# Kernel optimization log

Measured on AMD Instinct MI355X. Metric: run time of the kernel, lower is better.

The kernel has to match this reference:

```python
import jax, jax.numpy as jnp
import numpy as np

H, W, C = 96, 96, 21
THETA_ALPHA, THETA_BETA, THETA_GAMMA = 8.0, 0.125, 3.0
NUM_ITERATIONS = 5


def setup_inputs() -> dict:
    key = jax.random.key(0)
    k1, k2, k3, k4, k5 = jax.random.split(key, 5)
    unaries = jax.random.normal(k1, (1, H, W, C), dtype=jnp.float32)
    reference_image = jax.random.uniform(k2, (1, H, W, 3), dtype=jnp.float32)
    # truncated normal(mean=0, std=0.1) as in tf.initializers.truncated_normal
    spatial_ker_weights = 0.1 * jax.random.truncated_normal(k3, -2.0, 2.0, (C,), dtype=jnp.float32)
    bilateral_ker_weights = 0.1 * jax.random.truncated_normal(k4, -2.0, 2.0, (C,), dtype=jnp.float32)
    compatibility_matrix = 0.1 * jax.random.truncated_normal(k5, -2.0, 2.0, (C, C), dtype=jnp.float32)
    return {
        "unaries": unaries,
        "reference_image": reference_image,
        "spatial_ker_weights": spatial_ker_weights,
        "bilateral_ker_weights": bilateral_ker_weights,
        "compatibility_matrix": compatibility_matrix,
    }


def _gaussian_kernel(feats):
    # feats: [B, N, D] -> K[b, i, j] = exp(-0.5 * ||f_i - f_j||^2)
    sq = jnp.sum(feats * feats, axis=-1)  # [B, N]
    d2 = sq[:, :, None] + sq[:, None, :] - 2.0 * jnp.einsum("bnd,bmd->bnm", feats, feats)
    return jnp.exp(-0.5 * jnp.maximum(d2, 0.0))


def _build_kernels(reference_image):
    # Exact-math equivalent of the permutohedral lattice Gaussian filter:
    # spatial features = positions/theta_gamma; bilateral = [pos/theta_alpha, rgb/theta_beta].
    B = reference_image.shape[0]
    yy, xx = jnp.meshgrid(jnp.arange(H, dtype=jnp.float32), jnp.arange(W, dtype=jnp.float32), indexing="ij")
    pos = jnp.stack([yy, xx], axis=-1).reshape(1, H * W, 2)  # [1, N, 2]
    pos = jnp.broadcast_to(pos, (B, H * W, 2))
    col = reference_image.reshape(B, H * W, 3)
    k_spatial = _gaussian_kernel(pos / THETA_GAMMA)
    k_bilateral = _gaussian_kernel(jnp.concatenate([pos / THETA_ALPHA, col / THETA_BETA], axis=-1))
    return k_spatial, k_bilateral


def reference(unaries, reference_image, spatial_ker_weights, bilateral_ker_weights, compatibility_matrix):
    B = unaries.shape[0]
    N = H * W
    k_spatial, k_bilateral = _build_kernels(reference_image)  # built once; reused each iteration
    u = unaries.reshape(B, N, C)
    q = u
    for _ in range(NUM_ITERATIONS):
        q = jax.nn.softmax(q, axis=-1)
        spatial_out = jnp.einsum("bnm,bmc->bnc", k_spatial, q)
        bilateral_out = jnp.einsum("bnm,bmc->bnc", k_bilateral, q)
        # pairwise^T = compat @ diag(w_s) @ S^T + compat @ diag(w_b) @ Bi^T
        # => pairwise = (S * w_s + Bi * w_b) @ compat^T
        message = spatial_out * spatial_ker_weights + bilateral_out * bilateral_ker_weights
        pairwise = message @ compatibility_matrix.T
        q = u - pairwise
    return q.reshape(unaries.shape)
```

## Files before the change

kernel.cpp:

```cpp
#include <hip/hip_runtime.h>
#include <hip/hip_bf16.h>
#include <algorithm>
#include <cmath>

#define HH 96
#define WW 96
#define CC 21
#define NN (HH*WW)
#define NELEM (NN*CC)
#define RS 20
#define NPAR (2*CC + CC*CC)
#define L2E 1.4426950408889634f
#define MSTEPS 24
#define NBB (36*24)
#define NSTRIP 8
#define NBLUR (CC*NSTRIP)
#define SROWS 12
#define TRUNC2 1225
#define BLURKEY 0x10000

typedef short bf16x8 __attribute__((ext_vector_type(8)));
typedef float f32x16 __attribute__((ext_vector_type(16)));

__device__ __forceinline__ float fexp2(float x) { return __builtin_amdgcn_exp2f(x); }
__device__ __forceinline__ float fexp(float x)  { return __builtin_amdgcn_exp2f(x * L2E); }

__device__ __forceinline__ short f2b(float f) {
    __hip_bfloat16 h = __float2bfloat16(f);
    short s; __builtin_memcpy(&s, &h, 2); return s;
}

__global__ void k_sniff(const unsigned short* __restrict__ u16, int* __restrict__ flag32) {
    __shared__ int sfound;
    if (threadIdx.x == 0) sfound = 0;
    __syncthreads();
    const int base = blockIdx.x * (NELEM/32);
    int found = 0;
    for (int i = base + threadIdx.x; i < base + NELEM/32; i += 256) {
        unsigned v = u16[i];
        if ((v & 0x7F80u) == 0x7F80u) found = 1;
    }
    if (found) sfound = 1;
    __syncthreads();
    if (threadIdx.x == 0) flag32[blockIdx.x] = sfound;
}

__device__ __forceinline__ int rdflag(const int* __restrict__ flag32) {
    int f = 0;
    #pragma unroll
    for (int i = 0; i < 32; i++) f |= flag32[i];
    return f;
}

__global__ __launch_bounds__(256) void k_prep(
    const void* __restrict__ u, const void* __restrict__ img,
    const void* __restrict__ wS, const void* __restrict__ wB,
    const void* __restrict__ compat, const int* __restrict__ flag32,
    float* __restrict__ uf, float* __restrict__ featx, float* __restrict__ par,
    float* __restrict__ bil, __hip_bfloat16* __restrict__ pT)
{
    const int f = rdflag(flag32);
    const int tid = threadIdx.x;
    const int n = blockIdx.x * 256 + tid;

    if (blockIdx.x == 0) {
        for (int i = tid; i < NPAR; i += 256) {
            const void* src; int j;
            if (i < CC)        { src = wS;     j = i; }
            else if (i < 2*CC) { src = wB;     j = i - CC; }
            else               { src = compat; j = i - 2*CC; }
            par[i] = f ? ((const float*)src)[j]
                       : __bfloat162float(((const __hip_bfloat16*)src)[j]);
        }
    }

    {
        float c0, c1, c2;
        if (f) { const float* p = (const float*)img;
                 c0 = p[3*n]; c1 = p[3*n+1]; c2 = p[3*n+2]; }
        else   { const __hip_bfloat16* p = (const __hip_bfloat16*)img;
                 c0 = __bfloat162float(p[3*n]); c1 = __bfloat162float(p[3*n+1]);
                 c2 = __bfloat162float(p[3*n+2]); }
        float ym = (float)(n / WW), xm = (float)(n % WW);
        const float sc = 0.15014029f;
        const float cf = 9.6089787f;
        featx[8*n + 0] = -L2E * (fmaf(ym, ym, xm*xm) * 0.0078125f
                                 + 32.f * (c0*c0 + c1*c1 + c2*c2));
        featx[8*n + 1] = sc * ym;
        featx[8*n + 2] = sc * xm;
        featx[8*n + 3] = cf * c0;
        featx[8*n + 4] = cf * c1;
        featx[8*n + 5] = cf * c2;
        featx[8*n + 6] = 0.f;
        featx[8*n + 7] = 0.f;
    }

    float v[CC];
    float mx = -1e30f;
    #pragma unroll
    for (int c = 0; c < CC; c++) {
        float uv = f ? ((const float*)u)[n*CC + c]
                     : __bfloat162float(((const __hip_bfloat16*)u)[n*CC + c]);
        uf[n*CC + c] = uv;
        v[c] = uv;
        mx = fmaxf(mx, uv);
    }
    float s = 0.f;
    #pragma unroll
    for (int c = 0; c < CC; c++) { v[c] = fexp(v[c] - mx); s += v[c]; }
    float inv = 1.f / s;
    #pragma unroll
    for (int c = 0; c < CC; c++) {
        pT[(size_t)c*NN + n] = __float2bfloat16(v[c] * inv);
        bil[(size_t)c*NN + n] = 0.f;
    }
}

__global__ __launch_bounds__(256) void k_work(
    const __hip_bfloat16* __restrict__ pT,
    const float* __restrict__ featx,
    float* __restrict__ bil,
    float* __restrict__ s2T,
    const int* __restrict__ tab)
{
    __shared__ float smem[6176];
    const int tid = threadIdx.x;
    const int item = tab[blockIdx.x];

    if (item < BLURKEY) {
        float* lds_h = smem;
        const int wv   = tid >> 6, lane = tid & 63;
        const int quad = lane >> 5, lid = lane & 31;

        const int nt = item >> 5, mc = item & 31;
        const int ny0 = (nt / 6) * 16, nx0 = (nt % 6) * 16;
        const int my0 = (mc & 3) * 24, mx0 = (mc >> 2) * 16;

        const int dx = (mx0 > nx0 + 15) ? mx0 - (nx0 + 15)
                     : ((nx0 > mx0 + 15) ? nx0 - (mx0 + 15) : 0);
        const int lim = TRUNC2 - dx * dx;
        int T = (int)sqrtf((float)lim);
        T -= (T * T > lim);
        T += ((T + 1) * (T + 1) <= lim);

        int blo = ny0 - T - my0;      blo = blo < 0 ? 0 : blo;
        int bhi = ny0 + 15 + T - my0; bhi = bhi > 23 ? 23 : bhi;

        {
            float4* dst = (float4*)lds_h;
            for (int i = blo * 32 + tid; i < (bhi + 1) * 32; i += 256) {
                const int seg = i >> 5, off = i & 31;
                dst[i] = ((const float4*)(featx +
                          (size_t)((my0 + seg) * WW + mx0) * 8))[off];
            }
        }
        __syncthreads();

        const int by0 = ny0 + 4 * wv;
        int lo = by0 - T - my0;     lo = lo < 0 ? 0 : lo;
        int hi = by0 + 3 + T - my0; hi = hi > 23 ? 23 : hi;
        if (lo > hi) return;

        const int row = lid >> 4, col = lid & 15;
        const int n0 = (by0 + row) * WW + nx0 + col;
        const int n1 = n0 + 2 * WW;
        const float4 g0a = *(const float4*)(featx + (size_t)n0 * 8);
        const float4 g0b = *(const float4*)(featx + (size_t)n0 * 8 + 4);
        const float4 g1a = *(const float4*)(featx + (size_t)n1 * 8);
        const float4 g1b = *(const float4*)(featx + (size_t)n1 * 8 + 4);

        f32x16 acc0, acc1;
        #pragma unroll
        for (int r = 0; r < 16; r++) { acc0[r] = 0.f; acc1[r] = 0.f; }

        int mg = (my0 + lo) * WW + mx0 + quad * 8;
        #pragma unroll 1
        for (int step = lo; step <= hi; step++, mg += WW) {
            bf16x8 afrag = *(const bf16x8*)(pT + (size_t)lid * NN + mg);

            const float* h = lds_h + (step * 16 + quad * 8) * 8;
            float kb0[8], kb1[8];
            #pragma unroll
            for (int j = 0; j < 8; j++) {
                float4 ha = *(const float4*)(h + j * 8);
                float4 hb = *(const float4*)(h + j * 8 + 4);
                float s0 = g0a.x + ha.x;
                s0 = fmaf(g0a.y, ha.y, s0);
                s0 = fmaf(g0a.z, ha.z, s0);
                s0 = fmaf(g0a.w, ha.w, s0);
                s0 = fmaf(g0b.x, hb.x, s0);
                s0 = fmaf(g0b.y, hb.y, s0);
                kb0[j] = fexp2(s0);
                float s1 = g1a.x + ha.x;
                s1 = fmaf(g1a.y, ha.y, s1);
                s1 = fmaf(g1a.z, ha.z, s1);
                s1 = fmaf(g1a.w, ha.w, s1);
                s1 = fmaf(g1b.x, hb.x, s1);
                s1 = fmaf(g1b.y, hb.y, s1);
                kb1[j] = fexp2(s1);
            }
            bf16x8 b0, b1;
            #pragma unroll
            for (int j = 0; j < 8; j++) { b0[j] = f2b(kb0[j]); b1[j] = f2b(kb1[j]); }

            acc0 = __builtin_amdgcn_mfma_f32_32x32x16_bf16(afrag, b0, acc0, 0, 0, 0);
            acc1 = __builtin_amdgcn_mfma_f32_32x32x16_bf16(afrag, b1, acc1, 0, 0, 0);
        }

        #pragma unroll
        for (int r = 0; r < 16; r++) {
            int c = (r & 3) + 8 * (r >> 2) + 4 * quad;
            if (c < CC) {
                atomicAdd(&bil[(size_t)c * NN + n0], acc0[r]);
                atomicAdd(&bil[(size_t)c * NN + n1], acc1[r]);
            }
        }
    } else {
        __shared__ float w_s[RS + 1];
        float* A  = smem;
        float* B2 = smem + 4992;

        const int b2 = item - BLURKEY;
        const int c = b2 % CC;
        const int strip = b2 / CC;
        const int y0 = strip * SROWS;
        const int ylo = (y0 - RS < 0) ? 0 : y0 - RS;
        const int yhi = (y0 + SROWS - 1 + RS > HH - 1) ? HH - 1 : y0 + SROWS - 1 + RS;
        const int nrows = yhi - ylo + 1;

        if (tid <= RS) w_s[tid] = fexp2(-(float)(tid*tid) * (L2E / 18.f));
        const __hip_bfloat16* src = pT + (size_t)c * NN + ylo * WW;
        for (int i = tid; i < nrows * WW; i += 256)
            A[i] = __bfloat162float(src[i]);
        __syncthreads();

        for (int i = tid; i < SROWS * WW; i += 256) {
            const int yo = y0 + i / WW;
            const int x  = i % WW;
            float acc = A[(yo - ylo) * WW + x];
            #pragma unroll
            for (int d = 1; d <= RS; d++) {
                float s = 0.f;
                if (yo - d >= 0)  s += A[(yo - d - ylo) * WW + x];
                if (yo + d < HH)  s += A[(yo + d - ylo) * WW + x];
                acc = fmaf(w_s[d], s, acc);
            }
            B2[i] = acc;
        }
        __syncthreads();

        for (int i = tid; i < SROWS * WW; i += 256) {
            const int r = i / WW, x = i % WW;
            float acc = B2[i];
            #pragma unroll
            for (int d = 1; d <= RS; d++) {
                float s = 0.f;
                if (x - d >= 0)  s += B2[r * WW + x - d];
                if (x + d < WW)  s += B2[r * WW + x + d];
                acc = fmaf(w_s[d], s, acc);
            }
            s2T[(size_t)c * NN + (y0 + r) * WW + x] = acc;
        }
    }
}

__global__ __launch_bounds__(256) void k_update(
    float* __restrict__ bil, const float* __restrict__ s2T,
    const float* __restrict__ uf, const float* __restrict__ par,
    const int* __restrict__ flag32,
    __hip_bfloat16* __restrict__ pT, void* __restrict__ out, int last)
{
    __shared__ float sc[CC*CC + 1];
    __shared__ float sws[CC], swb[CC];
    const int tid = threadIdx.x;
    for (int i = tid; i < CC*CC; i += 256) sc[i] = par[2*CC + i];
    if (tid == 0) sc[CC*CC] = 0.f;
    if (tid < CC) { sws[tid] = par[tid]; swb[tid] = par[CC + tid]; }
    __syncthreads();

    const int half = tid & 1;
    const int n = blockIdx.x * 128 + (tid >> 1);

    float msg[11];
    #pragma unroll
    for (int k = 0; k < 11; k++) {
        const int cp = 2*k + half;
        if (cp < CC) {
            msg[k] = fmaf(s2T[(size_t)cp*NN + n], sws[cp],
                          bil[(size_t)cp*NN + n] * swb[cp]);
            bil[(size_t)cp*NN + n] = 0.f;
        } else msg[k] = 0.f;
    }

    float pw[CC];
    #pragma unroll
    for (int c = 0; c < CC; c++) {
        float a = msg[0] * sc[c*CC + half];
        #pragma unroll
        for (int k = 1; k < 11; k++)
            a = fmaf(msg[k], sc[c*CC + 2*k + half], a);
        pw[c] = a;
    }
    #pragma unroll
    for (int c = 0; c < CC; c++)
        pw[c] += __shfl_xor(pw[c], 1, 64);

    float qv[CC];
    float mx = -1e30f;
    #pragma unroll
    for (int c = 0; c < CC; c++) {
        qv[c] = uf[(size_t)n*CC + c] - pw[c];
        mx = fmaxf(mx, qv[c]);
    }

    if (last) {
        const int is_f32 = rdflag(flag32);
        #pragma unroll
        for (int k = 0; k < 11; k++) {
            const int ce = 2*k, co = (k < 10) ? 2*k + 1 : 0;
            float v = half ? qv[co] : qv[ce];
            const int c = 2*k + half;
            if (c < CC) {
                if (is_f32) ((float*)out)[(size_t)n*CC + c] = v;
                else ((__hip_bfloat16*)out)[(size_t)n*CC + c] = __float2bfloat16(v);
            }
        }
    } else {
        float ex[11]; float ssum = 0.f;
        #pragma unroll
        for (int k = 0; k < 11; k++) {
            const int ce = 2*k, co = (k < 10) ? 2*k + 1 : 0;
            float v = half ? qv[co] : qv[ce];
            float e = fexp(v - mx);
            if (2*k + half < CC) ssum += e;
            ex[k] = e;
        }
        ssum += __shfl_xor(ssum, 1, 64);
        const float inv = 1.f / ssum;
        #pragma unroll
        for (int k = 0; k < 11; k++) {
            const int c = 2*k + half;
            if (c < CC) pT[(size_t)c*NN + n] = __float2bfloat16(ex[k] * inv);
        }
    }
}

extern "C" void kernel_launch(void* const* d_in, const int* in_sizes, int n_in,
                              void* d_out, int out_size, void* d_ws, size_t ws_size,
                              hipStream_t stream)
{
    static int h_tab[NBB + NBLUR];
    static int h_n = 0;
    if (h_n == 0) {
        struct It { int key; int cost; };
        static It its[NBB + NBLUR];
        int m = 0;
        for (int nt = 0; nt < 36; nt++)
            for (int mc = 0; mc < 24; mc++) {
                const int ny0 = (nt / 6) * 16, nx0 = (nt % 6) * 16;
                const int my0 = (mc & 3) * 24, mx0 = (mc >> 2) * 16;
                const int dx = (mx0 > nx0 + 15) ? mx0 - (nx0 + 15)
                             : ((nx0 > mx0 + 15) ? nx0 - (mx0 + 15) : 0);
                const int lim = TRUNC2 - dx * dx;
                if (lim < 0) continue;
                int T = (int)std::sqrt((double)lim);
                while (T * T > lim) T--;
                while ((T + 1) * (T + 1) <= lim) T++;
                int cost = 0;
                for (int wv = 0; wv < 4; wv++) {
                    const int by0 = ny0 + 4 * wv;
                    int lo = by0 - T - my0;     if (lo < 0)  lo = 0;
                    int hi = by0 + 3 + T - my0; if (hi > 23) hi = 23;
                    if (lo <= hi) cost += hi - lo + 1;
                }
                if (cost == 0) continue;
                its[m].key = (nt << 5) | mc; its[m].cost = cost; m++;
            }
        for (int b = 0; b < NBLUR; b++) { its[m].key = BLURKEY + b; its[m].cost = 20; m++; }
        std::sort(its, its + m, [](const It& a, const It& b) { return a.cost > b.cost; });
        for (int i = 0; i < m; i++) h_tab[i] = its[i].key;
        h_n = m;
    }

    float* ws = (float*)d_ws;
    int*   flag32 = (int*)ws;
    float* par    = ws + 32;
    float* featx  = ws + 544;
    __hip_bfloat16* pT = (__hip_bfloat16*)(ws + 74272);
    float* uf  = ws + 74272 + 147456;
    float* s2T = uf + NELEM;
    float* bil = s2T + NELEM;
    int*   d_tab = (int*)(bil + NELEM);

    hipMemcpyAsync(d_tab, h_tab, h_n * sizeof(int), hipMemcpyHostToDevice, stream);

    k_sniff<<<32, 256, 0, stream>>>((const unsigned short*)d_in[0], flag32);
    k_prep<<<NN/256, 256, 0, stream>>>(d_in[0], d_in[1], d_in[2], d_in[3], d_in[4],
                                       flag32, uf, featx, par, bil, pT);

    for (int it = 0; it < 5; it++) {
        k_work<<<h_n, 256, 0, stream>>>(pT, featx, bil, s2T, d_tab);
        k_update<<<NN/128, 256, 0, stream>>>(bil, s2T, uf, par, flag32,
                                             pT, d_out, (it == 4) ? 1 : 0);
    }
}
```

Measured before the change: 237.9 us.

## Fuse all stages into one persistent cooperative kernel with grid syncs

Replaces the sniff, prep, and ten per-iteration work/update kernel launches with a single cooperative persistent kernel. Stages are separated by grid-wide barriers, and blocks loop over the work table and update chunks. The goal is to remove launch gaps and per-kernel ramp-up across the eleven small launches. In exchange, the grid is capped by occupancy (launch bounds 256,3), so work items are processed in loops instead of being fully spread across the device. Grid.sync also adds its own cost.

After: 574.5 us. 2.42x slower.

```diff
diff --git a/kernel.cpp b/kernel.cpp
--- a/kernel.cpp
+++ b/kernel.cpp
@@ -1,7 +1,10 @@
 #include <hip/hip_runtime.h>
+#include <hip/hip_cooperative_groups.h>
 #include <hip/hip_bf16.h>
 #include <algorithm>
 #include <cmath>
+
+namespace cg = cooperative_groups;
 
 #define HH 96
 #define WW 96
@@ -11,13 +14,12 @@
 #define RS 20
 #define NPAR (2*CC + CC*CC)
 #define L2E 1.4426950408889634f
-#define MSTEPS 24
 #define NBB (36*24)
-#define NSTRIP 8
-#define NBLUR (CC*NSTRIP)
+#define NBLUR (CC*8)
 #define SROWS 12
 #define TRUNC2 1225
 #define BLURKEY 0x10000
+#define NUPD (NN/128)
 
 typedef short bf16x8 __attribute__((ext_vector_type(8)));
 typedef float f32x16 __attribute__((ext_vector_type(16)));
@@ -30,318 +32,282 @@
     short s; __builtin_memcpy(&s, &h, 2); return s;
 }
 
-__global__ void k_sniff(const unsigned short* __restrict__ u16, int* __restrict__ flag32) {
-    __shared__ int sfound;
-    if (threadIdx.x == 0) sfound = 0;
-    __syncthreads();
-    const int base = blockIdx.x * (NELEM/32);
-    int found = 0;
-    for (int i = base + threadIdx.x; i < base + NELEM/32; i += 256) {
-        unsigned v = u16[i];
-        if ((v & 0x7F80u) == 0x7F80u) found = 1;
-    }
-    if (found) sfound = 1;
-    __syncthreads();
-    if (threadIdx.x == 0) flag32[blockIdx.x] = sfound;
-}
-
-__device__ __forceinline__ int rdflag(const int* __restrict__ flag32) {
+__global__ __launch_bounds__(256, 3) void k_all(
+    const void* __restrict__ u, const void* __restrict__ img,
+    const void* __restrict__ wS, const void* __restrict__ wB,
+    const void* __restrict__ compat, void* __restrict__ out,
+    float* __restrict__ uf, float* __restrict__ featx, float* __restrict__ par,
+    float* __restrict__ bil, __hip_bfloat16* __restrict__ pTg,
+    float* __restrict__ s2T, int* __restrict__ flag32,
+    const int* __restrict__ tab, int ntab)
+{
+    __shared__ float smem[6176];
+    cg::grid_group grid = cg::this_grid();
+    const int tid = threadIdx.x;
+    const int bid0 = blockIdx.x;
+    const int gsz = gridDim.x;
+
+    if (bid0 < 32) {
+        int* sf = (int*)smem;
+        if (tid == 0) *sf = 0;
+        __syncthreads();
+        const unsigned short* u16 = (const unsigned short*)u;
+        const int base = bid0 * (NELEM/32);
+        int found = 0;
+        for (int i = base + tid; i < base + NELEM/32; i += 256)
+            if ((u16[i] & 0x7F80u) == 0x7F80u) found = 1;
+        if (found) *sf = 1;
+        __syncthreads();
+        if (tid == 0) flag32[bid0] = *sf;
+    }
+    grid.sync();
+
     int f = 0;
     #pragma unroll
     for (int i = 0; i < 32; i++) f |= flag32[i];
-    return f;
-}
-
-__global__ __launch_bounds__(256) void k_prep(
-    const void* __restrict__ u, const void* __restrict__ img,
-    const void* __restrict__ wS, const void* __restrict__ wB,
-    const void* __restrict__ compat, const int* __restrict__ flag32,
-    float* __restrict__ uf, float* __restrict__ featx, float* __restrict__ par,
-    float* __restrict__ bil, __hip_bfloat16* __restrict__ pT)
-{
-    const int f = rdflag(flag32);
-    const int tid = threadIdx.x;
-    const int n = blockIdx.x * 256 + tid;
-
-    if (blockIdx.x == 0) {
-        for (int i = tid; i < NPAR; i += 256) {
-            const void* src; int j;
-            if (i < CC)        { src = wS;     j = i; }
-            else if (i < 2*CC) { src = wB;     j = i - CC; }
-            else               { src = compat; j = i - 2*CC; }
-            par[i] = f ? ((const float*)src)[j]
-                       : __bfloat162float(((const __hip_bfloat16*)src)[j]);
-        }
-    }
-
-    {
-        float c0, c1, c2;
-        if (f) { const float* p = (const float*)img;
-                 c0 = p[3*n]; c1 = p[3*n+1]; c2 = p[3*n+2]; }
-        else   { const __hip_bfloat16* p = (const __hip_bfloat16*)img;
-                 c0 = __bfloat162float(p[3*n]); c1 = __bfloat162float(p[3*n+1]);
-                 c2 = __bfloat162float(p[3*n+2]); }
-        float ym = (float)(n / WW), xm = (float)(n % WW);
-        const float sc = 0.15014029f;
-        const float cf = 9.6089787f;
-        featx[8*n + 0] = -L2E * (fmaf(ym, ym, xm*xm) * 0.0078125f
-                                 + 32.f * (c0*c0 + c1*c1 + c2*c2));
-        featx[8*n + 1] = sc * ym;
-        featx[8*n + 2] = sc * xm;
-        featx[8*n + 3] = cf * c0;
-        featx[8*n + 4] = cf * c1;
-        featx[8*n + 5] = cf * c2;
-        featx[8*n + 6] = 0.f;
-        featx[8*n + 7] = 0.f;
-    }
-
-    float v[CC];
-    float mx = -1e30f;
-    #pragma unroll
-    for (int c = 0; c < CC; c++) {
-        float uv = f ? ((const float*)u)[n*CC + c]
-                     : __bfloat162float(((const __hip_bfloat16*)u)[n*CC + c]);
-        uf[n*CC + c] = uv;
-        v[c] = uv;
-        mx = fmaxf(mx, uv);
-    }
-    float s = 0.f;
-    #pragma unroll
-    for (int c = 0; c < CC; c++) { v[c] = fexp(v[c] - mx); s += v[c]; }
-    float inv = 1.f / s;
-    #pragma unroll
-    for (int c = 0; c < CC; c++) {
-        pT[(size_t)c*NN + n] = __float2bfloat16(v[c] * inv);
-        bil[(size_t)c*NN + n] = 0.f;
-    }
-}
-
-__global__ __launch_bounds__(256) void k_work(
-    const __hip_bfloat16* __restrict__ pT,
-    const float* __restrict__ featx,
-    float* __restrict__ bil,
-    float* __restrict__ s2T,
-    const int* __restrict__ tab)
-{
-    __shared__ float smem[6176];
-    const int tid = threadIdx.x;
-    const int item = tab[blockIdx.x];
-
-    if (item < BLURKEY) {
-        float* lds_h = smem;
-        const int wv   = tid >> 6, lane = tid & 63;
-        const int quad = lane >> 5, lid = lane & 31;
-
-        const int nt = item >> 5, mc = item & 31;
-        const int ny0 = (nt / 6) * 16, nx0 = (nt % 6) * 16;
-        const int my0 = (mc & 3) * 24, mx0 = (mc >> 2) * 16;
-
-        const int dx = (mx0 > nx0 + 15) ? mx0 - (nx0 + 15)
-                     : ((nx0 > mx0 + 15) ? nx0 - (mx0 + 15) : 0);
-        const int lim = TRUNC2 - dx * dx;
-        int T = (int)sqrtf((float)lim);
-        T -= (T * T > lim);
-        T += ((T + 1) * (T + 1) <= lim);
-
-        int blo = ny0 - T - my0;      blo = blo < 0 ? 0 : blo;
-        int bhi = ny0 + 15 + T - my0; bhi = bhi > 23 ? 23 : bhi;
-
+
+    for (int ch = bid0; ch < 36; ch += gsz) {
+        const int n = ch * 256 + tid;
+        if (ch == 0) {
+            for (int i = tid; i < NPAR; i += 256) {
+                const void* src; int j;
+                if (i < CC)        { src = wS;     j = i; }
+                else if (i < 2*CC) { src = wB;     j = i - CC; }
+                else               { src = compat; j = i - 2*CC; }
+                par[i] = f ? ((const float*)src)[j]
+                           : __bfloat162float(((const __hip_bfloat16*)src)[j]);
+            }
+        }
         {
-            float4* dst = (float4*)lds_h;
-            for (int i = blo * 32 + tid; i < (bhi + 1) * 32; i += 256) {
-                const int seg = i >> 5, off = i & 31;
-                dst[i] = ((const float4*)(featx +
-                          (size_t)((my0 + seg) * WW + mx0) * 8))[off];
-            }
-        }
-        __syncthreads();
-
-        const int by0 = ny0 + 4 * wv;
-        int lo = by0 - T - my0;     lo = lo < 0 ? 0 : lo;
-        int hi = by0 + 3 + T - my0; hi = hi > 23 ? 23 : hi;
-        if (lo > hi) return;
-
-        const int row = lid >> 4, col = lid & 15;
-        const int n0 = (by0 + row) * WW + nx0 + col;
-        const int n1 = n0 + 2 * WW;
-        const float4 g0a = *(const float4*)(featx + (size_t)n0 * 8);
-        const float4 g0b = *(const float4*)(featx + (size_t)n0 * 8 + 4);
-        const float4 g1a = *(const float4*)(featx + (size_t)n1 * 8);
-        const float4 g1b = *(const float4*)(featx + (size_t)n1 * 8 + 4);
-
-        f32x16 acc0, acc1;
+            float c0, c1, c2;
+            if (f) { const float* p = (const float*)img;
+                     c0 = p[3*n]; c1 = p[3*n+1]; c2 = p[3*n+2]; }
+            else   { const __hip_bfloat16* p = (const __hip_bfloat16*)img;
+                     c0 = __bfloat162float(p[3*n]); c1 = __bfloat162float(p[3*n+1]);
+                     c2 = __bfloat162float(p[3*n+2]); }
+            float ym = (float)(n / WW), xm = (float)(n % WW);
+            const float sc_ = 0.15014029f;
+            const float cf  = 9.6089787f;
+            featx[8*n+0] = -L2E * (fmaf(ym, ym, xm*xm) * 0.0078125f
+                                   + 32.f * (c0*c0 + c1*c1 + c2*c2));
+            featx[8*n+1] = sc_*ym; featx[8*n+2] = sc_*xm;
+            featx[8*n+3] = cf*c0;  featx[8*n+4] = cf*c1;  featx[8*n+5] = cf*c2;
+            featx[8*n+6] = 0.f;    featx[8*n+7] = 0.f;
+        }
+        float v[CC]; float mx = -1e30f;
         #pragma unroll
-        for (int r = 0; r < 16; r++) { acc0[r] = 0.f; acc1[r] = 0.f; }
-
-        int mg = (my0 + lo) * WW + mx0 + quad * 8;
-        #pragma unroll 1
-        for (int step = lo; step <= hi; step++, mg += WW) {
-            bf16x8 afrag = *(const bf16x8*)(pT + (size_t)lid * NN + mg);
-
-            const float* h = lds_h + (step * 16 + quad * 8) * 8;
-            float kb0[8], kb1[8];
+        for (int c = 0; c < CC; c++) {
+            float uv = f ? ((const float*)u)[n*CC+c]
+                         : __bfloat162float(((const __hip_bfloat16*)u)[n*CC+c]);
+            uf[n*CC+c] = uv; v[c] = uv; mx = fmaxf(mx, uv);
+        }
+        float s = 0.f;
+        #pragma unroll
+        for (int c = 0; c < CC; c++) { v[c] = fexp(v[c]-mx); s += v[c]; }
+        float inv = 1.f/s;
+        #pragma unroll
+        for (int c = 0; c < CC; c++) {
+            pTg[(size_t)c*NN+n] = __float2bfloat16(v[c]*inv);
+            bil[(size_t)c*NN+n] = 0.f;
+        }
+    }
+    grid.sync();
+
+    for (int it = 0; it < 5; it++) {
+        for (int w = bid0; w < ntab; w += gsz) {
+            __syncthreads();
+            const int item = tab[w];
+            if (item < BLURKEY) {
+                float* lds_h = smem;
+                const int wv = tid >> 6, lane = tid & 63;
+                const int quad = lane >> 5, lid = lane & 31;
+                const int nt = item >> 5, mc = item & 31;
+                const int ny0 = (nt/6)*16, nx0 = (nt%6)*16;
+                const int my0 = (mc&3)*24, mx0 = (mc>>2)*16;
+                const int dx = (mx0 > nx0+15) ? mx0-(nx0+15)
+                             : ((nx0 > mx0+15) ? nx0-(mx0+15) : 0);
+                const int lim = TRUNC2 - dx*dx;
+                int T = (int)sqrtf((float)lim);
+                T -= (T*T > lim);
+                T += ((T+1)*(T+1) <= lim);
+                int blo = ny0 - T - my0;      blo = blo < 0 ? 0 : blo;
+                int bhi = ny0 + 15 + T - my0; bhi = bhi > 23 ? 23 : bhi;
+                {
+                    float4* dst = (float4*)lds_h;
+                    for (int i = blo*32 + tid; i < (bhi+1)*32; i += 256) {
+                        const int seg = i >> 5, off = i & 31;
+                        dst[i] = ((const float4*)(featx +
+                                  (size_t)((my0+seg)*WW + mx0)*8))[off];
+                    }
+                }
+                __syncthreads();
+                const int by0 = ny0 + 4*wv;
+                int lo = by0 - T - my0;     lo = lo < 0 ? 0 : lo;
+                int hi = by0 + 3 + T - my0; hi = hi > 23 ? 23 : hi;
+                if (lo <= hi) {
+                    const int row = lid >> 4, col = lid & 15;
+                    const int n0 = (by0+row)*WW + nx0 + col;
+                    const int n1 = n0 + 2*WW;
+                    const float4 g0a = *(const float4*)(featx + (size_t)n0*8);
+                    const float4 g0b = *(const float4*)(featx + (size_t)n0*8 + 4);
+                    const float4 g1a = *(const float4*)(featx + (size_t)n1*8);
+                    const float4 g1b = *(const float4*)(featx + (size_t)n1*8 + 4);
+                    f32x16 acc0, acc1;
+                    #pragma unroll
+                    for (int r = 0; r < 16; r++) { acc0[r]=0.f; acc1[r]=0.f; }
+                    int mg = (my0+lo)*WW + mx0 + quad*8;
+                    #pragma unroll 1
+                    for (int step = lo; step <= hi; step++, mg += WW) {
+                        bf16x8 afrag = *(const bf16x8*)(pTg + (size_t)lid*NN + mg);
+                        const float* h = lds_h + (step*16 + quad*8)*8;
+                        float kb0[8], kb1[8];
+                        #pragma unroll
+                        for (int j = 0; j < 8; j++) {
+                            float4 ha = *(const float4*)(h + j*8);
+                            float4 hb = *(const float4*)(h + j*8 + 4);
+                            float s0 = g0a.x + ha.x;
+                            s0 = fmaf(g0a.y,ha.y,s0); s0 = fmaf(g0a.z,ha.z,s0);
+                            s0 = fmaf(g0a.w,ha.w,s0); s0 = fmaf(g0b.x,hb.x,s0);
+                            s0 = fmaf(g0b.y,hb.y,s0);
+                            kb0[j] = fexp2(s0);
+                            float s1 = g1a.x + ha.x;
+                            s1 = fmaf(g1a.y,ha.y,s1); s1 = fmaf(g1a.z,ha.z,s1);
+                            s1 = fmaf(g1a.w,ha.w,s1); s1 = fmaf(g1b.x,hb.x,s1);
+                            s1 = fmaf(g1b.y,hb.y,s1);
+                            kb1[j] = fexp2(s1);
+                        }
+                        bf16x8 b0, b1;
+                        #pragma unroll
+                        for (int j = 0; j < 8; j++) { b0[j]=f2b(kb0[j]); b1[j]=f2b(kb1[j]); }
+                        acc0 = __builtin_amdgcn_mfma_f32_32x32x16_bf16(afrag,b0,acc0,0,0,0);
+                        acc1 = __builtin_amdgcn_mfma_f32_32x32x16_bf16(afrag,b1,acc1,0,0,0);
+                    }
+                    #pragma unroll
+                    for (int r = 0; r < 16; r++) {
+                        int c = (r&3) + 8*(r>>2) + 4*quad;
+                        if (c < CC) {
+                            atomicAdd(&bil[(size_t)c*NN + n0], acc0[r]);
+                            atomicAdd(&bil[(size_t)c*NN + n1], acc1[r]);
+                        }
+                    }
+                }
+            } else {
+                float* A   = smem;
+                float* B2  = smem + 4992;
+                float* w_s = smem + 6144;
+                const int b2 = item - BLURKEY;
+                const int c = b2 % CC;
+                const int strip = b2 / CC;
+                const int y0 = strip * SROWS;
+                const int ylo = (y0-RS < 0) ? 0 : y0-RS;
+                const int yhi = (y0+SROWS-1+RS > HH-1) ? HH-1 : y0+SROWS-1+RS;
+                const int nrows = yhi - ylo + 1;
+                if (tid <= RS) w_s[tid] = fexp2(-(float)(tid*tid)*(L2E/18.f));
+                const __hip_bfloat16* src = pTg + (size_t)c*NN + ylo*WW;
+                for (int i = tid; i < nrows*WW; i += 256)
+                    A[i] = __bfloat162float(src[i]);
+                __syncthreads();
+                for (int i = tid; i < SROWS*WW; i += 256) {
+                    const int yo = y0 + i/WW;
+                    const int x  = i % WW;
+                    float acc = A[(yo-ylo)*WW + x];
+                    #pragma unroll
+                    for (int d = 1; d <= RS; d++) {
+                        float s = 0.f;
+                        if (yo-d >= 0) s += A[(yo-d-ylo)*WW + x];
+                        if (yo+d < HH) s += A[(yo+d-ylo)*WW + x];
+                        acc = fmaf(w_s[d], s, acc);
+                    }
+                    B2[i] = acc;
+                }
+                __syncthreads();
+                for (int i = tid; i < SROWS*WW; i += 256) {
+                    const int r = i/WW, x = i%WW;
+                    float acc = B2[i];
+                    #pragma unroll
+                    for (int d = 1; d <= RS; d++) {
+                        float s = 0.f;
+                        if (x-d >= 0) s += B2[r*WW + x-d];
+                        if (x+d < WW) s += B2[r*WW + x+d];
+                        acc = fmaf(w_s[d], s, acc);
+                    }
+                    s2T[(size_t)c*NN + (y0+r)*WW + x] = acc;
+                }
+            }
+        }
+        grid.sync();
+
+        const int last = (it == 4);
+        for (int w = bid0; w < NUPD; w += gsz) {
+            __syncthreads();
+            float* sc  = smem;
+            float* sws = smem + 448;
+            float* swb = smem + 472;
+            for (int i = tid; i < CC*CC; i += 256) sc[i] = par[2*CC + i];
+            if (tid == 0) sc[CC*CC] = 0.f;
+            if (tid < CC) { sws[tid] = par[tid]; swb[tid] = par[CC+tid]; }
+            __syncthreads();
+            const int half = tid & 1;
+            const int n = w*128 + (tid >> 1);
+            float msg[11];
             #pragma unroll
-            for (int j = 0; j < 8; j++) {
-                float4 ha = *(const float4*)(h + j * 8);
-                float4 hb = *(const float4*)(h + j * 8 + 4);
-                float s0 = g0a.x + ha.x;
-                s0 = fmaf(g0a.y, ha.y, s0);
-                s0 = fmaf(g0a.z, ha.z, s0);
-                s0 = fmaf(g0a.w, ha.w, s0);
-                s0 = fmaf(g0b.x, hb.x, s0);
-                s0 = fmaf(g0b.y, hb.y, s0);
-                kb0[j] = fexp2(s0);
-                float s1 = g1a.x + ha.x;
-                s1 = fmaf(g1a.y, ha.y, s1);
-                s1 = fmaf(g1a.z, ha.z, s1);
-                s1 = fmaf(g1a.w, ha.w, s1);
-                s1 = fmaf(g1b.x, hb.x, s1);
-                s1 = fmaf(g1b.y, hb.y, s1);
-                kb1[j] = fexp2(s1);
-            }
-            bf16x8 b0, b1;
+            for (int k = 0; k < 11; k++) {
+                const int cp = 2*k + half;
+                if (cp < CC) {
+                    msg[k] = fmaf(s2T[(size_t)cp*NN+n], sws[cp],
+                                  bil[(size_t)cp*NN+n] * swb[cp]);
+                    bil[(size_t)cp*NN+n] = 0.f;
+                } else msg[k] = 0.f;
+            }
+            float pw[CC];
             #pragma unroll
-            for (int j = 0; j < 8; j++) { b0[j] = f2b(kb0[j]); b1[j] = f2b(kb1[j]); }
-
-            acc0 = __builtin_amdgcn_mfma_f32_32x32x16_bf16(afrag, b0, acc0, 0, 0, 0);
-            acc1 = __builtin_amdgcn_mfma_f32_32x32x16_bf16(afrag, b1, acc1, 0, 0, 0);
-        }
-
-        #pragma unroll
-        for (int r = 0; r < 16; r++) {
-            int c = (r & 3) + 8 * (r >> 2) + 4 * quad;
-            if (c < CC) {
-                atomicAdd(&bil[(size_t)c * NN + n0], acc0[r]);
-                atomicAdd(&bil[(size_t)c * NN + n1], acc1[r]);
-            }
-        }
-    } else {
-        __shared__ float w_s[RS + 1];
-        float* A  = smem;
-        float* B2 = smem + 4992;
-
-        const int b2 = item - BLURKEY;
-        const int c = b2 % CC;
-        const int strip = b2 / CC;
-        const int y0 = strip * SROWS;
-        const int ylo = (y0 - RS < 0) ? 0 : y0 - RS;
-        const int yhi = (y0 + SROWS - 1 + RS > HH - 1) ? HH - 1 : y0 + SROWS - 1 + RS;
-        const int nrows = yhi - ylo + 1;
-
-        if (tid <= RS) w_s[tid] = fexp2(-(float)(tid*tid) * (L2E / 18.f));
-        const __hip_bfloat16* src = pT + (size_t)c * NN + ylo * WW;
-        for (int i = tid; i < nrows * WW; i += 256)
-            A[i] = __bfloat162float(src[i]);
-        __syncthreads();
-
-        for (int i = tid; i < SROWS * WW; i += 256) {
-            const int yo = y0 + i / WW;
-            const int x  = i % WW;
-            float acc = A[(yo - ylo) * WW + x];
+            for (int c = 0; c < CC; c++) {
+                float a = msg[0] * sc[c*CC + half];
+                #pragma unroll
+                for (int k = 1; k < 11; k++)
+                    a = fmaf(msg[k], sc[c*CC + 2*k + half], a);
+                pw[c] = a;
+            }
             #pragma unroll
-            for (int d = 1; d <= RS; d++) {
-                float s = 0.f;
-                if (yo - d >= 0)  s += A[(yo - d - ylo) * WW + x];
-                if (yo + d < HH)  s += A[(yo + d - ylo) * WW + x];
-                acc = fmaf(w_s[d], s, acc);
-            }
-            B2[i] = acc;
-        }
-        __syncthreads();
-
-        for (int i = tid; i < SROWS * WW; i += 256) {
-            const int r = i / WW, x = i % WW;
-            float acc = B2[i];
+            for (int c = 0; c < CC; c++)
+                pw[c] += __shfl_xor(pw[c], 1, 64);
+            float qv[CC]; float mx = -1e30f;
             #pragma unroll
-            for (int d = 1; d <= RS; d++) {
-                float s = 0.f;
-                if (x - d >= 0)  s += B2[r * WW + x - d];
-                if (x + d < WW)  s += B2[r * WW + x + d];
-                acc = fmaf(w_s[d], s, acc);
-            }
-            s2T[(size_t)c * NN + (y0 + r) * WW + x] = acc;
-        }
-    }
-}
-
-__global__ __launch_bounds__(256) void k_update(
-    float* __restrict__ bil, const float* __restrict__ s2T,
-    const float* __restrict__ uf, const float* __restrict__ par,
-    const int* __restrict__ flag32,
-    __hip_bfloat16* __restrict__ pT, void* __restrict__ out, int last)
-{
-    __shared__ float sc[CC*CC + 1];
-    __shared__ float sws[CC], swb[CC];
-    const int tid = threadIdx.x;
-    for (int i = tid; i < CC*CC; i += 256) sc[i] = par[2*CC + i];
-    if (tid == 0) sc[CC*CC] = 0.f;
-    if (tid < CC) { sws[tid] = par[tid]; swb[tid] = par[CC + tid]; }
-    __syncthreads();
-
-    const int half = tid & 1;
-    const int n = blockIdx.x * 128 + (tid >> 1);
-
-    float msg[11];
-    #pragma unroll
-    for (int k = 0; k < 11; k++) {
-        const int cp = 2*k + half;
-        if (cp < CC) {
-            msg[k] = fmaf(s2T[(size_t)cp*NN + n], sws[cp],
-                          bil[(size_t)cp*NN + n] * swb[cp]);
-            bil[(size_t)cp*NN + n] = 0.f;
-        } else msg[k] = 0.f;
-    }
-
-    float pw[CC];
-    #pragma unroll
-    for (int c = 0; c < CC; c++) {
-        float a = msg[0] * sc[c*CC + half];
-        #pragma unroll
-        for (int k = 1; k < 11; k++)
-            a = fmaf(msg[k], sc[c*CC + 2*k + half], a);
-        pw[c] = a;
-    }
-    #pragma unroll
-    for (int c = 0; c < CC; c++)
-        pw[c] += __shfl_xor(pw[c], 1, 64);
-
-    float qv[CC];
-    float mx = -1e30f;
-    #pragma unroll
-    for (int c = 0; c < CC; c++) {
-        qv[c] = uf[(size_t)n*CC + c] - pw[c];
-        mx = fmaxf(mx, qv[c]);
-    }
-
-    if (last) {
-        const int is_f32 = rdflag(flag32);
-        #pragma unroll
-        for (int k = 0; k < 11; k++) {
-            const int ce = 2*k, co = (k < 10) ? 2*k + 1 : 0;
-            float v = half ? qv[co] : qv[ce];
-            const int c = 2*k + half;
-            if (c < CC) {
-                if (is_f32) ((float*)out)[(size_t)n*CC + c] = v;
-                else ((__hip_bfloat16*)out)[(size_t)n*CC + c] = __float2bfloat16(v);
-            }
-        }
-    } else {
-        float ex[11]; float ssum = 0.f;
-        #pragma unroll
-        for (int k = 0; k < 11; k++) {
-            const int ce = 2*k, co = (k < 10) ? 2*k + 1 : 0;
-            float v = half ? qv[co] : qv[ce];
-            float e = fexp(v - mx);
-            if (2*k + half < CC) ssum += e;
-            ex[k] = e;
-        }
-        ssum += __shfl_xor(ssum, 1, 64);
-        const float inv = 1.f / ssum;
-        #pragma unroll
-        for (int k = 0; k < 11; k++) {
-            const int c = 2*k + half;
-            if (c < CC) pT[(size_t)c*NN + n] = __float2bfloat16(ex[k] * inv);
-        }
+            for (int c = 0; c < CC; c++) {
+                qv[c] = uf[(size_t)n*CC+c] - pw[c];
+                mx = fmaxf(mx, qv[c]);
+            }
+            if (last) {
+                #pragma unroll
+                for (int k = 0; k < 11; k++) {
+                    const int ce = 2*k, co = (k < 10) ? 2*k+1 : 0;
+                    float v = half ? qv[co] : qv[ce];
+                    const int c = 2*k + half;
+                    if (c < CC) {
+                        if (f) ((float*)out)[(size_t)n*CC+c] = v;
+                        else ((__hip_bfloat16*)out)[(size_t)n*CC+c] = __float2bfloat16(v);
+                    }
+                }
+            } else {
+                float ex[11]; float ssum = 0.f;
+                #pragma unroll
+                for (int k = 0; k < 11; k++) {
+                    const int ce = 2*k, co = (k < 10) ? 2*k+1 : 0;
+                    float v = half ? qv[co] : qv[ce];
+                    float e = fexp(v - mx);
+                    if (2*k + half < CC) ssum += e;
+                    ex[k] = e;
+                }
+                ssum += __shfl_xor(ssum, 1, 64);
+                const float inv = 1.f/ssum;
+                #pragma unroll
+                for (int k = 0; k < 11; k++) {
+                    const int c = 2*k + half;
+                    if (c < CC) pTg[(size_t)c*NN+n] = __float2bfloat16(ex[k]*inv);
+                }
+            }
+        }
+        if (it != 4) grid.sync();
     }
 }
 
@@ -351,24 +317,25 @@
 {
     static int h_tab[NBB + NBLUR];
     static int h_n = 0;
+    static int G = 0;
     if (h_n == 0) {
         struct It { int key; int cost; };
         static It its[NBB + NBLUR];
         int m = 0;
         for (int nt = 0; nt < 36; nt++)
             for (int mc = 0; mc < 24; mc++) {
-                const int ny0 = (nt / 6) * 16, nx0 = (nt % 6) * 16;
-                const int my0 = (mc & 3) * 24, mx0 = (mc >> 2) * 16;
-                const int dx = (mx0 > nx0 + 15) ? mx0 - (nx0 + 15)
-                             : ((nx0 > mx0 + 15) ? nx0 - (mx0 + 15) : 0);
-                const int lim = TRUNC2 - dx * dx;
+                const int ny0 = (nt/6)*16, nx0 = (nt%6)*16;
+                const int my0 = (mc&3)*24, mx0 = (mc>>2)*16;
+                const int dx = (mx0 > nx0+15) ? mx0-(nx0+15)
+                             : ((nx0 > mx0+15) ? nx0-(mx0+15) : 0);
+                const int lim = TRUNC2 - dx*dx;
                 if (lim < 0) continue;
                 int T = (int)std::sqrt((double)lim);
-                while (T * T > lim) T--;
-                while ((T + 1) * (T + 1) <= lim) T++;
+                while (T*T > lim) T--;
+                while ((T+1)*(T+1) <= lim) T++;
                 int cost = 0;
                 for (int wv = 0; wv < 4; wv++) {
-                    const int by0 = ny0 + 4 * wv;
+                    const int by0 = ny0 + 4*wv;
                     int lo = by0 - T - my0;     if (lo < 0)  lo = 0;
                     int hi = by0 + 3 + T - my0; if (hi > 23) hi = 23;
                     if (lo <= hi) cost += hi - lo + 1;
@@ -380,6 +347,14 @@
         std::sort(its, its + m, [](const It& a, const It& b) { return a.cost > b.cost; });
         for (int i = 0; i < m; i++) h_tab[i] = its[i].key;
         h_n = m;
+    }
+    if (G == 0) {
+        int nb = 0;
+        if (hipOccupancyMaxActiveBlocksPerMultiprocessor(&nb, k_all, 256, 0) != hipSuccess
+            || nb < 1) nb = 3;
+        long cap = (long)nb * 256;
+        G = (int)std::min<long>(cap, (long)h_n);
+        if (G < NUPD) G = NUPD;
     }
 
     float* ws = (float*)d_ws;
@@ -394,13 +369,18 @@
 
     hipMemcpyAsync(d_tab, h_tab, h_n * sizeof(int), hipMemcpyHostToDevice, stream);
 
-    k_sniff<<<32, 256, 0, stream>>>((const unsigned short*)d_in[0], flag32);
-    k_prep<<<NN/256, 256, 0, stream>>>(d_in[0], d_in[1], d_in[2], d_in[3], d_in[4],
-                                       flag32, uf, featx, par, bil, pT);
-
-    for (int it = 0; it < 5; it++) {
-        k_work<<<h_n, 256, 0, stream>>>(pT, featx, bil, s2T, d_tab);
-        k_update<<<NN/128, 256, 0, stream>>>(bil, s2T, uf, par, flag32,
-                                             pT, d_out, (it == 4) ? 1 : 0);
-    }
+    const void* a_u   = d_in[0];
+    const void* a_img = d_in[1];
+    const void* a_wS  = d_in[2];
+    const void* a_wB  = d_in[3];
+    const void* a_cm  = d_in[4];
+    void*  a_out = d_out;
+    float* a_uf = uf; float* a_fx = featx; float* a_par = par;
+    float* a_bil = bil; __hip_bfloat16* a_pT = pT; float* a_s2T = s2T;
+    int* a_flag = flag32; const int* a_tab = d_tab; int a_n = h_n;
+    void* args[] = { &a_u, &a_img, &a_wS, &a_wB, &a_cm, &a_out,
+                     &a_uf, &a_fx, &a_par, &a_bil, &a_pT, &a_s2T,
+                     &a_flag, &a_tab, &a_n };
+
+    hipLaunchCooperativeKernel((void*)k_all, dim3(G), dim3(256), args, 0, stream);
 }
```

## Cache computed bilateral kernel tiles in workspace and reuse across iterations

Applied to the files above, without the earlier changes.

The first mean-field iteration computes the bilateral Gaussian kernel fragments in bf16 and writes them to a workspace buffer. Iterations two to five read those cached fragments instead of recomputing the exp and feature dot products. This trades ALU and exp work for extra global memory traffic on every later iteration. The cache is used only when the workspace is large enough, otherwise every iteration recomputes the kernel as before.

New measurement: 238.8 us. Within noise of the previous version (+0.4%).

```diff
diff --git a/kernel.cpp b/kernel.cpp
--- a/kernel.cpp
+++ b/kernel.cpp
@@ -11,10 +11,8 @@
 #define RS 20
 #define NPAR (2*CC + CC*CC)
 #define L2E 1.4426950408889634f
-#define MSTEPS 24
 #define NBB (36*24)
-#define NSTRIP 8
-#define NBLUR (CC*NSTRIP)
+#define NBLUR (CC*8)
 #define SROWS 12
 #define TRUNC2 1225
 #define BLURKEY 0x10000
@@ -52,6 +50,26 @@
     return f;
 }
 
+__device__ __forceinline__ void item_geom(int item, int& ny0, int& nx0, int& my0,
+                                          int& mx0, int& dx, int& T) {
+    const int nt = item >> 5, mc = item & 31;
+    ny0 = (nt / 6) * 16; nx0 = (nt % 6) * 16;
+    my0 = (mc & 3) * 24; mx0 = (mc >> 2) * 16;
+    dx = (mx0 > nx0 + 15) ? mx0 - (nx0 + 15)
+       : ((nx0 > mx0 + 15) ? nx0 - (mx0 + 15) : 0);
+    const int lim = TRUNC2 - dx * dx;
+    T = (int)sqrtf((float)lim);
+    T -= (T * T > lim);
+    T += ((T + 1) * (T + 1) <= lim);
+}
+
+__device__ __forceinline__ void wave_range(int ny0, int my0, int T, int wv,
+                                           int& lo, int& hi) {
+    const int by0 = ny0 + 4 * wv;
+    lo = by0 - T - my0;     lo = lo < 0 ? 0 : lo;
+    hi = by0 + 3 + T - my0; hi = hi > 23 ? 23 : hi;
+}
+
 __global__ __launch_bounds__(256) void k_prep(
     const void* __restrict__ u, const void* __restrict__ img,
     const void* __restrict__ wS, const void* __restrict__ wB,
@@ -73,7 +91,6 @@
                        : __bfloat162float(((const __hip_bfloat16*)src)[j]);
         }
     }
-
     {
         float c0, c1, c2;
         if (f) { const float* p = (const float*)img;
@@ -116,36 +133,75 @@
     }
 }
 
-__global__ __launch_bounds__(256) void k_work(
-    const __hip_bfloat16* __restrict__ pT,
-    const float* __restrict__ featx,
-    float* __restrict__ bil,
-    float* __restrict__ s2T,
-    const int* __restrict__ tab)
+__device__ __forceinline__ void blur_item(
+    int item, float* smem, const __hip_bfloat16* __restrict__ pT,
+    float* __restrict__ s2T, int tid)
+{
+    float* A   = smem;
+    float* B2  = smem + 4992;
+    float* w_s = smem + 6144;
+    const int b2 = item - BLURKEY;
+    const int c = b2 % CC;
+    const int strip = b2 / CC;
+    const int y0 = strip * SROWS;
+    const int ylo = (y0 - RS < 0) ? 0 : y0 - RS;
+    const int yhi = (y0 + SROWS - 1 + RS > HH - 1) ? HH - 1 : y0 + SROWS - 1 + RS;
+    const int nrows = yhi - ylo + 1;
+
+    if (tid <= RS) w_s[tid] = fexp2(-(float)(tid*tid) * (L2E / 18.f));
+    const __hip_bfloat16* src = pT + (size_t)c * NN + ylo * WW;
+    for (int i = tid; i < nrows * WW; i += 256)
+        A[i] = __bfloat162float(src[i]);
+    __syncthreads();
+
+    for (int i = tid; i < SROWS * WW; i += 256) {
+        const int yo = y0 + i / WW;
+        const int x  = i % WW;
+        float acc = A[(yo - ylo) * WW + x];
+        #pragma unroll
+        for (int d = 1; d <= RS; d++) {
+            float s = 0.f;
+            if (yo - d >= 0)  s += A[(yo - d - ylo) * WW + x];
+            if (yo + d < HH)  s += A[(yo + d - ylo) * WW + x];
+            acc = fmaf(w_s[d], s, acc);
+        }
+        B2[i] = acc;
+    }
+    __syncthreads();
+
+    for (int i = tid; i < SROWS * WW; i += 256) {
+        const int r = i / WW, x = i % WW;
+        float acc = B2[i];
+        #pragma unroll
+        for (int d = 1; d <= RS; d++) {
+            float s = 0.f;
+            if (x - d >= 0)  s += B2[r * WW + x - d];
+            if (x + d < WW)  s += B2[r * WW + x + d];
+            acc = fmaf(w_s[d], s, acc);
+        }
+        s2T[(size_t)c * NN + (y0 + r) * WW + x] = acc;
+    }
+}
+
+__global__ __launch_bounds__(256) void k_workK(
+    const __hip_bfloat16* __restrict__ pT, const float* __restrict__ featx,
+    float* __restrict__ bil, float* __restrict__ s2T,
+    const int* __restrict__ tab, short* __restrict__ kb)
 {
     __shared__ float smem[6176];
     const int tid = threadIdx.x;
-    const int item = tab[blockIdx.x];
+    const int item = tab[2*blockIdx.x];
+    const int base = tab[2*blockIdx.x + 1];
 
     if (item < BLURKEY) {
         float* lds_h = smem;
-        const int wv   = tid >> 6, lane = tid & 63;
+        const int wv = tid >> 6, lane = tid & 63;
         const int quad = lane >> 5, lid = lane & 31;
-
-        const int nt = item >> 5, mc = item & 31;
-        const int ny0 = (nt / 6) * 16, nx0 = (nt % 6) * 16;
-        const int my0 = (mc & 3) * 24, mx0 = (mc >> 2) * 16;
-
-        const int dx = (mx0 > nx0 + 15) ? mx0 - (nx0 + 15)
-                     : ((nx0 > mx0 + 15) ? nx0 - (mx0 + 15) : 0);
-        const int lim = TRUNC2 - dx * dx;
-        int T = (int)sqrtf((float)lim);
-        T -= (T * T > lim);
-        T += ((T + 1) * (T + 1) <= lim);
+        int ny0, nx0, my0, mx0, dx, T;
+        item_geom(item, ny0, nx0, my0, mx0, dx, T);
 
         int blo = ny0 - T - my0;      blo = blo < 0 ? 0 : blo;
         int bhi = ny0 + 15 + T - my0; bhi = bhi > 23 ? 23 : bhi;
-
         {
             float4* dst = (float4*)lds_h;
             for (int i = blo * 32 + tid; i < (bhi + 1) * 32; i += 256) {
@@ -156,13 +212,18 @@
         }
         __syncthreads();
 
-        const int by0 = ny0 + 4 * wv;
-        int lo = by0 - T - my0;     lo = lo < 0 ? 0 : lo;
-        int hi = by0 + 3 + T - my0; hi = hi > 23 ? 23 : hi;
+        int lo, hi;
+        wave_range(ny0, my0, T, wv, lo, hi);
         if (lo > hi) return;
+        int pre = 0;
+        for (int wv2 = 0; wv2 < wv; wv2++) {
+            int l2, h2; wave_range(ny0, my0, T, wv2, l2, h2);
+            if (l2 <= h2) pre += h2 - l2 + 1;
+        }
+        short* kp = kb + (((size_t)(base + pre)) << 10) + (lane << 3);
 
         const int row = lid >> 4, col = lid & 15;
-        const int n0 = (by0 + row) * WW + nx0 + col;
+        const int n0 = (ny0 + 4*wv + row) * WW + nx0 + col;
         const int n1 = n0 + 2 * WW;
         const float4 g0a = *(const float4*)(featx + (size_t)n0 * 8);
         const float4 g0b = *(const float4*)(featx + (size_t)n0 * 8 + 4);
@@ -175,9 +236,8 @@
 
         int mg = (my0 + lo) * WW + mx0 + quad * 8;
         #pragma unroll 1
-        for (int step = lo; step <= hi; step++, mg += WW) {
+        for (int step = lo; step <= hi; step++, mg += WW, kp += 1024) {
             bf16x8 afrag = *(const bf16x8*)(pT + (size_t)lid * NN + mg);
-
             const float* h = lds_h + (step * 16 + quad * 8) * 8;
             float kb0[8], kb1[8];
             #pragma unroll
@@ -185,17 +245,13 @@
                 float4 ha = *(const float4*)(h + j * 8);
                 float4 hb = *(const float4*)(h + j * 8 + 4);
                 float s0 = g0a.x + ha.x;
-                s0 = fmaf(g0a.y, ha.y, s0);
-                s0 = fmaf(g0a.z, ha.z, s0);
-                s0 = fmaf(g0a.w, ha.w, s0);
-                s0 = fmaf(g0b.x, hb.x, s0);
+                s0 = fmaf(g0a.y, ha.y, s0); s0 = fmaf(g0a.z, ha.z, s0);
+                s0 = fmaf(g0a.w, ha.w, s0); s0 = fmaf(g0b.x, hb.x, s0);
                 s0 = fmaf(g0b.y, hb.y, s0);
                 kb0[j] = fexp2(s0);
                 float s1 = g1a.x + ha.x;
-                s1 = fmaf(g1a.y, ha.y, s1);
-                s1 = fmaf(g1a.z, ha.z, s1);
-                s1 = fmaf(g1a.w, ha.w, s1);
-                s1 = fmaf(g1b.x, hb.x, s1);
+                s1 = fmaf(g1a.y, ha.y, s1); s1 = fmaf(g1a.z, ha.z, s1);
+                s1 = fmaf(g1a.w, ha.w, s1); s1 = fmaf(g1b.x, hb.x, s1);
                 s1 = fmaf(g1b.y, hb.y, s1);
                 kb1[j] = fexp2(s1);
             }
@@ -203,10 +259,12 @@
             #pragma unroll
             for (int j = 0; j < 8; j++) { b0[j] = f2b(kb0[j]); b1[j] = f2b(kb1[j]); }
 
+            *(bf16x8*)kp = b0;
+            *(bf16x8*)(kp + 512) = b1;
+
             acc0 = __builtin_amdgcn_mfma_f32_32x32x16_bf16(afrag, b0, acc0, 0, 0, 0);
             acc1 = __builtin_amdgcn_mfma_f32_32x32x16_bf16(afrag, b1, acc1, 0, 0, 0);
         }
-
         #pragma unroll
         for (int r = 0; r < 16; r++) {
             int c = (r & 3) + 8 * (r >> 2) + 4 * quad;
@@ -216,51 +274,61 @@
             }
         }
     } else {
-        __shared__ float w_s[RS + 1];
-        float* A  = smem;
-        float* B2 = smem + 4992;
-
-        const int b2 = item - BLURKEY;
-        const int c = b2 % CC;
-        const int strip = b2 / CC;
-        const int y0 = strip * SROWS;
-        const int ylo = (y0 - RS < 0) ? 0 : y0 - RS;
-        const int yhi = (y0 + SROWS - 1 + RS > HH - 1) ? HH - 1 : y0 + SROWS - 1 + RS;
-        const int nrows = yhi - ylo + 1;
-
-        if (tid <= RS) w_s[tid] = fexp2(-(float)(tid*tid) * (L2E / 18.f));
-        const __hip_bfloat16* src = pT + (size_t)c * NN + ylo * WW;
-        for (int i = tid; i < nrows * WW; i += 256)
-            A[i] = __bfloat162float(src[i]);
-        __syncthreads();
-
-        for (int i = tid; i < SROWS * WW; i += 256) {
-            const int yo = y0 + i / WW;
-            const int x  = i % WW;
-            float acc = A[(yo - ylo) * WW + x];
-            #pragma unroll
-            for (int d = 1; d <= RS; d++) {
-                float s = 0.f;
-                if (yo - d >= 0)  s += A[(yo - d - ylo) * WW + x];
-                if (yo + d < HH)  s += A[(yo + d - ylo) * WW + x];
-                acc = fmaf(w_s[d], s, acc);
-            }
-            B2[i] = acc;
-        }
-        __syncthreads();
-
-        for (int i = tid; i < SROWS * WW; i += 256) {
-            const int r = i / WW, x = i % WW;
-            float acc = B2[i];
-            #pragma unroll
-            for (int d = 1; d <= RS; d++) {
-                float s = 0.f;
-                if (x - d >= 0)  s += B2[r * WW + x - d];
-                if (x + d < WW)  s += B2[r * WW + x + d];
-                acc = fmaf(w_s[d], s, acc);
-            }
-            s2T[(size_t)c * NN + (y0 + r) * WW + x] = acc;
-        }
+        blur_item(item, smem, pT, s2T, tid);
+    }
+}
+
+__global__ __launch_bounds__(256) void k_workC(
+    const __hip_bfloat16* __restrict__ pT,
+    float* __restrict__ bil, float* __restrict__ s2T,
+    const int* __restrict__ tab, const short* __restrict__ kb)
+{
+    __shared__ float smem[6176];
+    const int tid = threadIdx.x;
+    const int item = tab[2*blockIdx.x];
+    const int base = tab[2*blockIdx.x + 1];
+
+    if (item < BLURKEY) {
+        const int wv = tid >> 6, lane = tid & 63;
+        const int quad = lane >> 5, lid = lane & 31;
+        int ny0, nx0, my0, mx0, dx, T;
+        item_geom(item, ny0, nx0, my0, mx0, dx, T);
+        int lo, hi;
+        wave_range(ny0, my0, T, wv, lo, hi);
+        if (lo > hi) return;
+        int pre = 0;
+        for (int wv2 = 0; wv2 < wv; wv2++) {
+            int l2, h2; wave_range(ny0, my0, T, wv2, l2, h2);
+            if (l2 <= h2) pre += h2 - l2 + 1;
+        }
+        const short* kp = kb + (((size_t)(base + pre)) << 10) + (lane << 3);
+
+        const int row = lid >> 4, col = lid & 15;
+        const int n0 = (ny0 + 4*wv + row) * WW + nx0 + col;
+        const int n1 = n0 + 2 * WW;
+
+        f32x16 acc0, acc1;
+        #pragma unroll
+        for (int r = 0; r < 16; r++) { acc0[r] = 0.f; acc1[r] = 0.f; }
+
+        int mg = (my0 + lo) * WW + mx0 + quad * 8;
+        for (int step = lo; step <= hi; step++, mg += WW, kp += 1024) {
+            bf16x8 afrag = *(const bf16x8*)(pT + (size_t)lid * NN + mg);
+            bf16x8 b0 = *(const bf16x8*)kp;
+            bf16x8 b1 = *(const bf16x8*)(kp + 512);
+            acc0 = __builtin_amdgcn_mfma_f32_32x32x16_bf16(afrag, b0, acc0, 0, 0, 0);
+            acc1 = __builtin_amdgcn_mfma_f32_32x32x16_bf16(afrag, b1, acc1, 0, 0, 0);
+        }
+        #pragma unroll
+        for (int r = 0; r < 16; r++) {
+            int c = (r & 3) + 8 * (r >> 2) + 4 * quad;
+            if (c < CC) {
+                atomicAdd(&bil[(size_t)c * NN + n0], acc0[r]);
+                atomicAdd(&bil[(size_t)c * NN + n1], acc1[r]);
+            }
+        }
+    } else {
+        blur_item(item, smem, pT, s2T, tid);
     }
 }
 
@@ -349,26 +417,27 @@
                               void* d_out, int out_size, void* d_ws, size_t ws_size,
                               hipStream_t stream)
 {
-    static int h_tab[NBB + NBLUR];
+    static int h_tab[2 * (NBB + NBLUR)];
     static int h_n = 0;
+    static long h_slots = 0;
     if (h_n == 0) {
         struct It { int key; int cost; };
         static It its[NBB + NBLUR];
         int m = 0;
         for (int nt = 0; nt < 36; nt++)
             for (int mc = 0; mc < 24; mc++) {
-                const int ny0 = (nt / 6) * 16, nx0 = (nt % 6) * 16;
-                const int my0 = (mc & 3) * 24, mx0 = (mc >> 2) * 16;
-                const int dx = (mx0 > nx0 + 15) ? mx0 - (nx0 + 15)
-                             : ((nx0 > mx0 + 15) ? nx0 - (mx0 + 15) : 0);
-                const int lim = TRUNC2 - dx * dx;
+                const int ny0 = (nt/6)*16, nx0 = (nt%6)*16;
+                const int my0 = (mc&3)*24, mx0 = (mc>>2)*16;
+                const int dx = (mx0 > nx0+15) ? mx0-(nx0+15)
+                             : ((nx0 > mx0+15) ? nx0-(mx0+15) : 0);
+                const int lim = TRUNC2 - dx*dx;
                 if (lim < 0) continue;
                 int T = (int)std::sqrt((double)lim);
-                while (T * T > lim) T--;
-                while ((T + 1) * (T + 1) <= lim) T++;
+                while (T*T > lim) T--;
+                while ((T+1)*(T+1) <= lim) T++;
                 int cost = 0;
                 for (int wv = 0; wv < 4; wv++) {
-                    const int by0 = ny0 + 4 * wv;
+                    const int by0 = ny0 + 4*wv;
                     int lo = by0 - T - my0;     if (lo < 0)  lo = 0;
                     int hi = by0 + 3 + T - my0; if (hi > 23) hi = 23;
                     if (lo <= hi) cost += hi - lo + 1;
@@ -378,8 +447,14 @@
             }
         for (int b = 0; b < NBLUR; b++) { its[m].key = BLURKEY + b; its[m].cost = 20; m++; }
         std::sort(its, its + m, [](const It& a, const It& b) { return a.cost > b.cost; });
-        for (int i = 0; i < m; i++) h_tab[i] = its[i].key;
+        long base = 0;
+        for (int i = 0; i < m; i++) {
+            h_tab[2*i] = its[i].key;
+            h_tab[2*i + 1] = (int)base;
+            if (its[i].key < BLURKEY) base += its[i].cost;
+        }
         h_n = m;
+        h_slots = base;
     }
 
     float* ws = (float*)d_ws;
@@ -391,15 +466,22 @@
     float* s2T = uf + NELEM;
     float* bil = s2T + NELEM;
     int*   d_tab = (int*)(bil + NELEM);
-
-    hipMemcpyAsync(d_tab, h_tab, h_n * sizeof(int), hipMemcpyHostToDevice, stream);
+    short* d_kb  = (short*)(ws + 806912);
+
+    const size_t need = 806912ull*4 + (size_t)h_slots * 2048ull;
+    const int use_cache = (ws_size >= need);
+
+    hipMemcpyAsync(d_tab, h_tab, 2 * h_n * sizeof(int), hipMemcpyHostToDevice, stream);
 
     k_sniff<<<32, 256, 0, stream>>>((const unsigned short*)d_in[0], flag32);
     k_prep<<<NN/256, 256, 0, stream>>>(d_in[0], d_in[1], d_in[2], d_in[3], d_in[4],
                                        flag32, uf, featx, par, bil, pT);
 
     for (int it = 0; it < 5; it++) {
-        k_work<<<h_n, 256, 0, stream>>>(pT, featx, bil, s2T, d_tab);
+        if (it == 0 || !use_cache)
+            k_workK<<<h_n, 256, 0, stream>>>(pT, featx, bil, s2T, d_tab, d_kb);
+        else
+            k_workC<<<h_n, 256, 0, stream>>>(pT, bil, s2T, d_tab, d_kb);
         k_update<<<NN/128, 256, 0, stream>>>(bil, s2T, uf, par, flag32,
                                              pT, d_out, (it == 4) ? 1 : 0);
     }
```
